# Kernel optimization log

Measured on AMD Instinct MI355X. Metric: run time of the kernel, lower is better.

The kernel has to match this reference:

```python
import jax, jax.numpy as jnp
import numpy as np

B, S, DIM, NL = 8, 1024, 1024, 2
EPS = 1e-5
# FeedForward hidden: int(2*(4*DIM)/3)=2730 -> round to multiple_of=256 -> 2816
FFN_HID = 2816


def _uniform(key, shape, k):
    return jax.random.uniform(key, shape, jnp.float32, -k, k)


def setup_inputs() -> dict:
    key = jax.random.key(0)
    ks = jax.random.split(key, 16)
    k = 1.0 / np.sqrt(DIM)
    inp = {
        'x': jax.random.normal(ks[0], (B, S, DIM), jnp.float32),
        'gru_norm_w': jnp.ones((DIM,), jnp.float32),
        # layer 0: input size DIM; layer 1: input size 2*DIM (bidirectional concat)
        'w_ih_l0': _uniform(ks[1], (2, 3 * DIM, DIM), k),
        'w_hh_l0': _uniform(ks[2], (2, 3 * DIM, DIM), k),
        'b_ih_l0': _uniform(ks[3], (2, 3 * DIM), k),
        'b_hh_l0': _uniform(ks[4], (2, 3 * DIM), k),
        'w_ih_l1': _uniform(ks[5], (2, 3 * DIM, 2 * DIM), k),
        'w_hh_l1': _uniform(ks[6], (2, 3 * DIM, DIM), k),
        'b_ih_l1': _uniform(ks[7], (2, 3 * DIM), k),
        'b_hh_l1': _uniform(ks[8], (2, 3 * DIM), k),
        'gru_out_w': _uniform(ks[9], (DIM, 2 * DIM), 1.0 / np.sqrt(2 * DIM)),
        'ffn_norm_w': jnp.ones((DIM,), jnp.float32),
        'w1': _uniform(ks[10], (FFN_HID, DIM), k),
        'w2': _uniform(ks[11], (DIM, FFN_HID), 1.0 / np.sqrt(FFN_HID)),
        'w3': _uniform(ks[12], (FFN_HID, DIM), k),
    }
    return inp


def rmsnorm(x, w, eps=EPS):
    return x * jax.lax.rsqrt(jnp.mean(x * x, axis=-1, keepdims=True) + eps) * w


def gru_dir(x, w_ih, w_hh, b_ih, b_hh, reverse):
    """One GRU direction. x: [B,S,Din] -> [B,S,H]. PyTorch gate order r,z,n."""
    H = w_hh.shape[1]
    # precompute input gates for all timesteps (big GEMM)
    xg = jnp.einsum('bsd,gd->bsg', x, w_ih) + b_ih        # [B,S,3H]
    xg = jnp.swapaxes(xg, 0, 1)                            # [S,B,3H]
    h0 = jnp.zeros((x.shape[0], H), x.dtype)

    def step(h, g):
        hg = h @ w_hh.T + b_hh                             # [B,3H]
        xr, xz, xn = jnp.split(g, 3, axis=-1)
        hr, hz, hn = jnp.split(hg, 3, axis=-1)
        r = jax.nn.sigmoid(xr + hr)
        z = jax.nn.sigmoid(xz + hz)
        n = jnp.tanh(xn + r * hn)
        h = (1.0 - z) * n + z * h
        return h, h

    _, ys = jax.lax.scan(step, h0, xg, reverse=reverse)    # outputs in input order
    return jnp.swapaxes(ys, 0, 1)                          # [B,S,H]


def reference(x, gru_norm_w, w_ih_l0, w_hh_l0, b_ih_l0, b_hh_l0,
              w_ih_l1, w_hh_l1, b_ih_l1, b_hh_l1,
              gru_out_w, ffn_norm_w, w1, w2, w3):
    h = rmsnorm(x, gru_norm_w)
    for wi, wh, bi, bh in ((w_ih_l0, w_hh_l0, b_ih_l0, b_hh_l0),
                           (w_ih_l1, w_hh_l1, b_ih_l1, b_hh_l1)):
        fwd = gru_dir(h, wi[0], wh[0], bi[0], bh[0], reverse=False)
        bwd = gru_dir(h, wi[1], wh[1], bi[1], bh[1], reverse=True)
        h = jnp.concatenate([fwd, bwd], axis=-1)           # [B,S,2*DIM]
    x = x + h @ gru_out_w.T                                # residual 1
    hn = rmsnorm(x, ffn_norm_w)
    ffn = (jax.nn.silu(hn @ w1.T) * (hn @ w3.T)) @ w2.T    # SwiGLU
    return x + ffn                                         # residual 2
```

## Files before the change

kernel.cpp:

```cpp
#include <hip/hip_runtime.h>
#include <stdint.h>


#define S_LEN 1024
#define NWG_DIR 64
#define HPW 16
#define WSTR 1032

typedef __attribute__((ext_vector_type(8))) __bf16 bf16x8;
typedef __attribute__((ext_vector_type(4))) float f32x4;

__device__ __forceinline__ float bf2f(unsigned short u) {
    union { unsigned int i; float f; } v; v.i = ((unsigned int)u) << 16; return v.f;
}
__device__ __forceinline__ unsigned short f2bf(float f) {
    unsigned int i = __float_as_uint(f);
    unsigned int r = (i + 0x7fffu + ((i >> 16) & 1u)) >> 16;
    return (unsigned short)r;
}
__device__ __forceinline__ bool dt_is_f32(const unsigned int* dt) {
    return dt[0] == 0x3F800000u;
}
__device__ __forceinline__ float ld_ext(const void* p, long i, bool f32) {
    return f32 ? ((const float*)p)[i] : bf2f(((const unsigned short*)p)[i]);
}
__device__ __forceinline__ void st8bf(unsigned short* d, float4 a, float4 b) {
    uint4 u;
    u.x = (unsigned)f2bf(a.x) | ((unsigned)f2bf(a.y) << 16);
    u.y = (unsigned)f2bf(a.z) | ((unsigned)f2bf(a.w) << 16);
    u.z = (unsigned)f2bf(b.x) | ((unsigned)f2bf(b.y) << 16);
    u.w = (unsigned)f2bf(b.z) | ((unsigned)f2bf(b.w) << 16);
    *(uint4*)d = u;
}
__device__ __forceinline__ void gload_lds16(const void* g, void* l) {
    __builtin_amdgcn_global_load_lds(
        (const __attribute__((address_space(1))) unsigned int*)g,
        (__attribute__((address_space(3))) unsigned int*)l, 16, 0, 0);
}
__device__ __forceinline__ unsigned int a_ld32(const unsigned int* p) {
    return __hip_atomic_load(p, __ATOMIC_RELAXED, __HIP_MEMORY_SCOPE_AGENT);
}
__device__ __forceinline__ unsigned long long a_ld64(const unsigned long long* p) {
    return __hip_atomic_load(p, __ATOMIC_RELAXED, __HIP_MEMORY_SCOPE_AGENT);
}
__device__ __forceinline__ void a_st32(unsigned int* p, unsigned int v) {
    __hip_atomic_store(p, v, __ATOMIC_RELAXED, __HIP_MEMORY_SCOPE_AGENT);
}

template <bool EXT_IN>
__global__ __launch_bounds__(256) void rmsnorm_k(const void* __restrict__ xin,
                                                 const void* __restrict__ w,
                                                 unsigned short* __restrict__ outp,
                                                 const unsigned int* __restrict__ dt) {
    const bool f32 = dt_is_f32(dt);
    const long row = blockIdx.x;
    const int tid = threadIdx.x;
    float v[4];
    if (!EXT_IN || f32) {
        const float* x = (const float*)xin + row * 1024 + tid * 4;
        f32x4 f = *(const f32x4*)x;
        v[0] = f[0]; v[1] = f[1]; v[2] = f[2]; v[3] = f[3];
    } else {
        const unsigned short* x = (const unsigned short*)xin + row * 1024 + tid * 4;
        uint2 u = *(const uint2*)x;
        v[0] = bf2f((unsigned short)(u.x & 0xffff)); v[1] = bf2f((unsigned short)(u.x >> 16));
        v[2] = bf2f((unsigned short)(u.y & 0xffff)); v[3] = bf2f((unsigned short)(u.y >> 16));
    }
    float ss = v[0]*v[0] + v[1]*v[1] + v[2]*v[2] + v[3]*v[3];
    for (int off = 32; off > 0; off >>= 1) ss += __shfl_down(ss, off, 64);
    __shared__ float red[4];
    __shared__ float bc;
    if ((tid & 63) == 0) red[tid >> 6] = ss;
    __syncthreads();
    if (tid == 0) bc = rsqrtf((red[0] + red[1] + red[2] + red[3]) * (1.f / 1024.f) + 1e-5f);
    __syncthreads();
    const float sc = bc;
    unsigned short o0 = f2bf(v[0] * sc * ld_ext(w, tid*4+0, f32));
    unsigned short o1 = f2bf(v[1] * sc * ld_ext(w, tid*4+1, f32));
    unsigned short o2 = f2bf(v[2] * sc * ld_ext(w, tid*4+2, f32));
    unsigned short o3 = f2bf(v[3] * sc * ld_ext(w, tid*4+3, f32));
    *(uint2*)(outp + row * 1024 + tid * 4) =
        make_uint2((unsigned int)o0 | ((unsigned int)o1 << 16),
                   (unsigned int)o2 | ((unsigned int)o3 << 16));
}

enum { EPI_NONE = 0, EPI_SILU = 1, EPI_MUL_I = 2, EPI_ADD_EXT = 3, EPI_ADD_F32 = 4 };
enum { OUT_BF16 = 0, OUT_F32 = 1, OUT_EXT = 2 };

template <int EPI, int OUTMODE, bool HAS_BIAS>
__global__ __launch_bounds__(256) void gemm_bt(const unsigned short* __restrict__ A,
                                               const void* __restrict__ W,
                                               const void* __restrict__ bias,
                                               const void* __restrict__ aux,
                                               void* __restrict__ Cout, int N, int K,
                                               const unsigned int* __restrict__ dt) {
    __shared__ __align__(16) unsigned short sA[128 * 32];
    __shared__ __align__(16) unsigned short sB[128 * 32];
    const bool f32 = dt_is_f32(dt);
    const int tid = threadIdx.x;
    const int lane = tid & 63;
    const int wave = tid >> 6;
    const int wm = (wave >> 1) * 64, wn = (wave & 1) * 64;
    const int lm = lane & 15, q = lane >> 4;
    const long rowA0 = (long)blockIdx.y * 128;
    const long rowB0 = (long)blockIdx.x * 128;
    const int r0 = tid >> 2, c0 = tid & 3;

    f32x4 acc[4][4] = {};

    for (int kt = 0; kt < K; kt += 32) {
        gload_lds16(A + (rowA0 + r0) * K + kt + c0 * 8, &sA[tid * 8]);
        gload_lds16(A + (rowA0 + r0 + 64) * K + kt + c0 * 8, &sA[(tid + 256) * 8]);
        if (!f32) {
            const unsigned short* Wb = (const unsigned short*)W;
            gload_lds16(Wb + (rowB0 + r0) * K + kt + c0 * 8, &sB[tid * 8]);
            gload_lds16(Wb + (rowB0 + r0 + 64) * K + kt + c0 * 8, &sB[(tid + 256) * 8]);
        } else {
            const float* Wf = (const float*)W;
            const float* p0 = Wf + (rowB0 + r0) * K + kt + c0 * 8;
            const float* p1 = Wf + (rowB0 + r0 + 64) * K + kt + c0 * 8;
            float4 a0 = *(const float4*)p0, a1 = *(const float4*)(p0 + 4);
            float4 b0 = *(const float4*)p1, b1 = *(const float4*)(p1 + 4);
            st8bf(&sB[tid * 8], a0, a1);
            st8bf(&sB[(tid + 256) * 8], b0, b1);
        }
        __syncthreads();
        bf16x8 af[4], bfr[4];
#pragma unroll
        for (int i = 0; i < 4; ++i) af[i] = *(const bf16x8*)&sA[(wm + i * 16 + lm) * 32 + q * 8];
#pragma unroll
        for (int j = 0; j < 4; ++j) bfr[j] = *(const bf16x8*)&sB[(wn + j * 16 + lm) * 32 + q * 8];
#pragma unroll
        for (int i = 0; i < 4; ++i)
#pragma unroll
            for (int j = 0; j < 4; ++j)
                acc[i][j] = __builtin_amdgcn_mfma_f32_16x16x32_bf16(af[i], bfr[j], acc[i][j], 0, 0, 0);
        __syncthreads();
    }

#pragma unroll
    for (int j = 0; j < 4; ++j) {
        const long col = rowB0 + wn + j * 16 + lm;
        float bv = 0.f;
        if (HAS_BIAS) bv = ld_ext(bias, col, f32);
#pragma unroll
        for (int i = 0; i < 4; ++i) {
#pragma unroll
            for (int r = 0; r < 4; ++r) {
                const long row = rowA0 + wm + i * 16 + q * 4 + r;
                const long idx = row * N + col;
                float v = acc[i][j][r] + bv;
                if (EPI == EPI_SILU)    v = v / (1.f + __expf(-v));
                if (EPI == EPI_MUL_I)   v *= bf2f(((const unsigned short*)aux)[idx]);
                if (EPI == EPI_ADD_EXT) v += ld_ext(aux, idx, f32);
                if (EPI == EPI_ADD_F32) v += ((const float*)aux)[idx];
                if (OUTMODE == OUT_F32)       ((float*)Cout)[idx] = v;
                else if (OUTMODE == OUT_BF16) ((unsigned short*)Cout)[idx] = f2bf(v);
                else { if (f32) ((float*)Cout)[idx] = v; else ((unsigned short*)Cout)[idx] = f2bf(v); }
            }
        }
    }
}

__global__ __launch_bounds__(256) void gru_recur(const unsigned short* __restrict__ xg,
                                                 const void* __restrict__ whh,
                                                 const void* __restrict__ bhh,
                                                 unsigned short* __restrict__ out,
                                                 unsigned short* __restrict__ hpp,
                                                 unsigned int* __restrict__ flags,
                                                 const unsigned int* __restrict__ dt) {
    extern __shared__ char smem[];
    unsigned short* w_lds = (unsigned short*)smem;
    unsigned short* h_lds = w_lds + 48 * WSTR;
    float* xg_lds = (float*)(h_lds + 16 * WSTR);
    float* red = xg_lds + 768;
    float* hstate = red + 3072;
    float* bhh_l = hstate + 128;
    unsigned short* hpub = (unsigned short*)(bhh_l + 48);

    const bool f32 = dt_is_f32(dt);
    const int tid = threadIdx.x;
    const int lane = tid & 63, wave = tid >> 6;
    const int dir = blockIdx.x >> 6;
    const int slot = blockIdx.x & 63;
    const int H0 = slot * HPW;
    const int lm = lane & 15, q = lane >> 4;
    unsigned int* fl = flags + dir * 64;

    for (int idx = tid; idx < 48 * 128; idx += 256) {
        int row = idx >> 7, seg = idx & 127;
        int gate = row >> 4, j = row & 15;
        size_t grow = (size_t)(dir * 3072 + gate * 1024 + H0 + j);
        if (!f32) {
            uint4 vv = *(const uint4*)((const unsigned short*)whh + grow * 1024 + seg * 8);
            *(uint4*)&w_lds[row * WSTR + seg * 8] = vv;
        } else {
            const float* wf = (const float*)whh + grow * 1024 + seg * 8;
            float4 a = *(const float4*)wf, b = *(const float4*)(wf + 4);
            st8bf(&w_lds[row * WSTR + seg * 8], a, b);
        }
    }
    if (tid < 48) {
        int gate = tid >> 4, j = tid & 15;
        bhh_l[tid] = ld_ext(bhh, dir * 3072 + gate * 1024 + H0 + j, f32);
    }
    if (tid < 128) hstate[tid] = 0.f;
    for (int i = tid; i < 16 * 128; i += 256) {
        int m = i >> 7, sg = i & 127;
        uint4 z = {0, 0, 0, 0};
        *(uint4*)&h_lds[m * WSTR + sg * 8] = z;
    }
    {
        int s0 = dir ? (S_LEN - 1) : 0;
        if (tid < 192) {
            int v0 = tid * 2, m = v0 / 48, c = v0 % 48;
            int gate = c >> 4, j = c & 15;
            unsigned int u = *(const unsigned int*)(xg + (size_t)(m * S_LEN + s0) * 6144 +
                                                   dir * 3072 + gate * 1024 + H0 + j);
            xg_lds[m * 48 + c] = bf2f((unsigned short)(u & 0xffff));
            xg_lds[m * 48 + c + 1] = bf2f((unsigned short)(u >> 16));
        }
    }

    unsigned short* hpp_d = hpp + (size_t)dir * 2 * 8 * 1024;
    unsigned int* hpp_u32 = (unsigned int*)hpp_d;
    const unsigned long long* hpp_u64 = (const unsigned long long*)hpp_d;

    for (int t = 0; t < S_LEN; ++t) {
        const int s = dir ? (S_LEN - 1 - t) : t;
        const int buf = t & 1;

        unsigned int nxt = 0;
        int nm = 0, nc = 0;
        const bool has_nxt = (t + 1 < S_LEN) && (tid < 192);
        if (has_nxt) {
            int sn = dir ? (S_LEN - 2 - t) : (t + 1);
            int v0 = tid * 2; nm = v0 / 48; nc = v0 % 48;
            int gate = nc >> 4, j = nc & 15;
            nxt = *(const unsigned int*)(xg + (size_t)(nm * S_LEN + sn) * 6144 +
                                         dir * 3072 + gate * 1024 + H0 + j);
        }
        if (t > 0) {
            if (wave == 0) {
                unsigned int f;
                do {
                    f = a_ld32(&fl[lane]);
                } while (__ballot(f < (unsigned int)t) != 0ULL);
            }
            __syncthreads();
            const unsigned long long* src = hpp_u64 + (size_t)((t - 1) & 1) * 2048;
#pragma unroll
            for (int i = 0; i < 8; ++i) {
                int idx = tid + i * 256;
                int m = idx >> 8, qw = idx & 255;
                unsigned long long v = a_ld64(src + m * 256 + qw);
                *(unsigned long long*)&h_lds[m * WSTR + qw * 4] = v;
            }
        }
        if (has_nxt) {
            xg_lds[(buf ^ 1) * 384 + nm * 48 + nc] = bf2f((unsigned short)(nxt & 0xffff));
            xg_lds[(buf ^ 1) * 384 + nm * 48 + nc + 1] = bf2f((unsigned short)(nxt >> 16));
        }
        __syncthreads();
        f32x4 pacc[3] = {};
#pragma unroll
        for (int kk = 0; kk < 8; ++kk) {
            const int k0 = (wave * 8 + kk) * 32 + q * 8;
            bf16x8 a = *(const bf16x8*)&h_lds[lm * WSTR + k0];
#pragma unroll
            for (int tl = 0; tl < 3; ++tl) {
                bf16x8 b = *(const bf16x8*)&w_lds[(tl * 16 + lm) * WSTR + k0];
                pacc[tl] = __builtin_amdgcn_mfma_f32_16x16x32_bf16(a, b, pacc[tl], 0, 0, 0);
            }
        }
#pragma unroll
        for (int tl = 0; tl < 3; ++tl)
            *(f32x4*)&red[((wave * 3 + tl) * 64 + lane) * 4] = pacc[tl];
        __syncthreads();
        if (tid < 128) {
            const int m = tid >> 4, hh = tid & 15;
            const int cl = (m >> 2) * 16 + hh, rg = m & 3;
            float rp = 0.f, zp = 0.f, np = 0.f;
#pragma unroll
            for (int wv = 0; wv < 4; ++wv) {
                rp += red[((wv * 3 + 0) * 64 + cl) * 4 + rg];
                zp += red[((wv * 3 + 1) * 64 + cl) * 4 + rg];
                np += red[((wv * 3 + 2) * 64 + cl) * 4 + rg];
            }
            const float* xb = &xg_lds[buf * 384 + m * 48];
            float rr = xb[hh] + rp + bhh_l[hh];
            float zz = xb[16 + hh] + zp + bhh_l[16 + hh];
            float hn_ = np + bhh_l[32 + hh];
            float rgate = 1.f / (1.f + __expf(-rr));
            float zgate = 1.f / (1.f + __expf(-zz));
            float ngate = tanhf(xb[32 + hh] + rgate * hn_);
            float hv = (1.f - zgate) * ngate + zgate * hstate[tid];
            hstate[tid] = hv;
            unsigned short hb = f2bf(hv);
            hpub[tid] = hb;
            out[(size_t)(m * S_LEN + s) * 2048 + dir * 1024 + H0 + hh] = hb;
        }
        __syncthreads();
        if (wave == 0) {
            unsigned int hw = *(const unsigned int*)&hpub[lane * 2];
            int m = lane >> 3, j = lane & 7;
            a_st32(hpp_u32 + ((size_t)buf * 8 + m) * 512 + (H0 >> 1) + j, hw);
            asm volatile("s_waitcnt vmcnt(0)" ::: "memory");
            if (lane == 0) a_st32(&fl[slot], (unsigned int)(t + 1));
        }
    }
}

extern "C" void kernel_launch(void* const* d_in, const int* in_sizes, int n_in,
                              void* d_out, int out_size, void* d_ws, size_t ws_size,
                              hipStream_t stream) {
    (void)in_sizes; (void)n_in; (void)out_size; (void)ws_size;
    const void* x    = d_in[0];
    const unsigned int* dt = (const unsigned int*)d_in[1];
    const void* gnw  = d_in[1];
    const void* wih0 = d_in[2];
    const void* whh0 = d_in[3];
    const void* bih0 = d_in[4];
    const void* bhh0 = d_in[5];
    const void* wih1 = d_in[6];
    const void* whh1 = d_in[7];
    const void* bih1 = d_in[8];
    const void* bhh1 = d_in[9];
    const void* gow  = d_in[10];
    const void* fnw  = d_in[11];
    const void* w1   = d_in[12];
    const void* w2   = d_in[13];
    const void* w3   = d_in[14];

    char* ws = (char*)d_ws;
    size_t o = 0;
    auto alloc = [&](size_t b) { size_t r = o; o += (b + 255) & ~(size_t)255; return r; };
    const size_t oFLG = alloc(2 * 2 * 64 * 4);
    const size_t oHPP = alloc((size_t)2 * 2 * 8 * 1024 * 2);
    const size_t oHN  = alloc((size_t)8192 * 1024 * 2);
    const size_t oXG  = alloc((size_t)8192 * 6144 * 2);
    const size_t oG0  = alloc((size_t)8192 * 2048 * 2);
    const size_t oG1  = alloc((size_t)8192 * 2048 * 2);

    unsigned int* flg    = (unsigned int*)(ws + oFLG);
    unsigned short* hpp  = (unsigned short*)(ws + oHPP);
    unsigned short* hnrm = (unsigned short*)(ws + oHN);
    unsigned short* xg   = (unsigned short*)(ws + oXG);
    unsigned short* g0   = (unsigned short*)(ws + oG0);
    unsigned short* g1   = (unsigned short*)(ws + oG1);
    unsigned short* act  = xg;
    unsigned short* gbuf = xg + (size_t)8192 * 2816;
    float* x1            = (float*)(ws + oG0);

    const size_t lds = (size_t)(48 + 16) * WSTR * 2 + (768 + 3072 + 128 + 48) * 4 + 256;
    (void)hipFuncSetAttribute(reinterpret_cast<const void*>(&gru_recur),
                              hipFuncAttributeMaxDynamicSharedMemorySize, (int)lds);

    hipMemsetAsync(ws + oFLG, 0, 2 * 2 * 64 * 4, stream);
    rmsnorm_k<true><<<8192, 256, 0, stream>>>(x, gnw, hnrm, dt);
    gemm_bt<EPI_NONE, OUT_BF16, true><<<dim3(48, 64), 256, 0, stream>>>(hnrm, wih0, bih0, nullptr, xg, 6144, 1024, dt);
    gru_recur<<<128, 256, lds, stream>>>(xg, whh0, bhh0, g0, hpp, flg, dt);
    gemm_bt<EPI_NONE, OUT_BF16, true><<<dim3(48, 64), 256, 0, stream>>>(g0, wih1, bih1, nullptr, xg, 6144, 2048, dt);
    gru_recur<<<128, 256, lds, stream>>>(xg, whh1, bhh1, g1, hpp, flg + 128, dt);
    gemm_bt<EPI_ADD_EXT, OUT_F32, false><<<dim3(8, 64), 256, 0, stream>>>(g1, gow, nullptr, x, x1, 1024, 2048, dt);
    rmsnorm_k<false><<<8192, 256, 0, stream>>>(x1, fnw, hnrm, dt);
    gemm_bt<EPI_SILU, OUT_BF16, false><<<dim3(22, 64), 256, 0, stream>>>(hnrm, w1, nullptr, nullptr, act, 2816, 1024, dt);
    gemm_bt<EPI_MUL_I, OUT_BF16, false><<<dim3(22, 64), 256, 0, stream>>>(hnrm, w3, nullptr, act, gbuf, 2816, 1024, dt);
    gemm_bt<EPI_ADD_F32, OUT_EXT, false><<<dim3(8, 64), 256, 0, stream>>>(gbuf, w2, nullptr, x1, d_out, 1024, 2816, dt);
}
```

Before: 10.45 ms.

## Replace GRU flag barrier with checksum-validated hidden-state publication and register-held weights

The persistent GRU recurrence no longer publishes hidden-state slices plus a separate per-workgroup flag that a waiting wave polls. Each workgroup now writes its slice together with a step-keyed hash, and readers spin until the hash matches, so one round-trip replaces a flag wait followed by a data load. W_hh fragments are also preloaded into registers instead of being read from LDS every step, tanh switches to an exp-based form, and the output store moves to a second wave. This cuts latency on the serial critical path, but the checksum scheme carries a small risk of false validation and the extra registers may cause spilling.

```diff
diff --git a/kernel.cpp b/kernel.cpp
--- a/kernel.cpp
+++ b/kernel.cpp
@@ -3,9 +3,9 @@
 
 
 #define S_LEN 1024
-#define NWG_DIR 64
 #define HPW 16
 #define WSTR 1032
+#define HASH_K 0x9E3779B1u
 
 typedef __attribute__((ext_vector_type(8))) __bf16 bf16x8;
 typedef __attribute__((ext_vector_type(4))) float f32x4;
@@ -45,6 +45,13 @@
 }
 __device__ __forceinline__ void a_st32(unsigned int* p, unsigned int v) {
     __hip_atomic_store(p, v, __ATOMIC_RELAXED, __HIP_MEMORY_SCOPE_AGENT);
+}
+__device__ __forceinline__ unsigned int rotl32(unsigned int x, int s) {
+    return (x << s) | (x >> ((32 - s) & 31));
+}
+__device__ __forceinline__ float fast_tanh(float x) {
+    float ex = __expf(2.f * x);
+    return 1.f - 2.f / (ex + 1.f);
 }
 
 template <bool EXT_IN>
@@ -162,13 +169,12 @@
     }
 }
 
-__global__ __launch_bounds__(256) void gru_recur(const unsigned short* __restrict__ xg,
-                                                 const void* __restrict__ whh,
-                                                 const void* __restrict__ bhh,
-                                                 unsigned short* __restrict__ out,
-                                                 unsigned short* __restrict__ hpp,
-                                                 unsigned int* __restrict__ flags,
-                                                 const unsigned int* __restrict__ dt) {
+__global__ __launch_bounds__(256, 1) void gru_recur(const unsigned short* __restrict__ xg,
+                                                    const void* __restrict__ whh,
+                                                    const void* __restrict__ bhh,
+                                                    unsigned short* __restrict__ out,
+                                                    unsigned int* __restrict__ hpp,
+                                                    const unsigned int* __restrict__ dt) {
     extern __shared__ char smem[];
     unsigned short* w_lds = (unsigned short*)smem;
     unsigned short* h_lds = w_lds + 48 * WSTR;
@@ -185,7 +191,7 @@
     const int slot = blockIdx.x & 63;
     const int H0 = slot * HPW;
     const int lm = lane & 15, q = lane >> 4;
-    unsigned int* fl = flags + dir * 64;
+    unsigned int* hppD = hpp + dir * (2 * 64 * 68);
 
     for (int idx = tid; idx < 48 * 128; idx += 256) {
         int row = idx >> 7, seg = idx & 127;
@@ -221,10 +227,15 @@
             xg_lds[m * 48 + c + 1] = bf2f((unsigned short)(u >> 16));
         }
     }
-
-    unsigned short* hpp_d = hpp + (size_t)dir * 2 * 8 * 1024;
-    unsigned int* hpp_u32 = (unsigned int*)hpp_d;
-    const unsigned long long* hpp_u64 = (const unsigned long long*)hpp_d;
+    __syncthreads();
+    bf16x8 wfrag[8][3];
+#pragma unroll
+    for (int kk = 0; kk < 8; ++kk)
+#pragma unroll
+        for (int tl = 0; tl < 3; ++tl)
+            wfrag[kk][tl] = *(const bf16x8*)&w_lds[(tl * 16 + lm) * WSTR + (wave * 8 + kk) * 32 + q * 8];
+
+    const int cp = tid >> 2, cr = tid & 3;
 
     for (int t = 0; t < S_LEN; ++t) {
         const int s = dir ? (S_LEN - 1 - t) : t;
@@ -241,21 +252,38 @@
                                          dir * 3072 + gate * 1024 + H0 + j);
         }
         if (t > 0) {
-            if (wave == 0) {
-                unsigned int f;
-                do {
-                    f = a_ld32(&fl[lane]);
-                } while (__ballot(f < (unsigned int)t) != 0ULL);
-            }
-            __syncthreads();
-            const unsigned long long* src = hpp_u64 + (size_t)((t - 1) & 1) * 2048;
-#pragma unroll
-            for (int i = 0; i < 8; ++i) {
-                int idx = tid + i * 256;
-                int m = idx >> 8, qw = idx & 255;
-                unsigned long long v = a_ld64(src + m * 256 + qw);
-                *(unsigned long long*)&h_lds[m * WSTR + qw * 4] = v;
-            }
+            const unsigned int hashv = (unsigned int)t * HASH_K;
+            const unsigned int* base = hppD + ((t - 1) & 1) * (64 * 68) + cp * 68;
+            const unsigned long long* srcq = (const unsigned long long*)(base) + cr * 8;
+            unsigned long long d[8];
+            int ok;
+            do {
+#pragma unroll
+                for (int k2 = 0; k2 < 8; ++k2) d[k2] = a_ld64(srcq + k2);
+                unsigned int cs = a_ld32(base + 64);
+                unsigned int x = 0;
+#pragma unroll
+                for (int k2 = 0; k2 < 8; ++k2) {
+                    int i0 = cr * 16 + 2 * k2;
+                    x ^= rotl32((unsigned int)d[k2], i0 & 31) ^
+                         rotl32((unsigned int)(d[k2] >> 32), (i0 + 1) & 31);
+                }
+                unsigned int sx = x ^ __shfl_xor(x, 1);
+                sx ^= __shfl_xor(sx, 2);
+                ok = ((sx ^ hashv) == cs);
+            } while (__syncthreads_count(ok) < 256);
+            uint4 w0 = { (unsigned int)d[0], (unsigned int)(d[0] >> 32),
+                         (unsigned int)d[1], (unsigned int)(d[1] >> 32) };
+            uint4 w1 = { (unsigned int)d[2], (unsigned int)(d[2] >> 32),
+                         (unsigned int)d[3], (unsigned int)(d[3] >> 32) };
+            uint4 w2 = { (unsigned int)d[4], (unsigned int)(d[4] >> 32),
+                         (unsigned int)d[5], (unsigned int)(d[5] >> 32) };
+            uint4 w3 = { (unsigned int)d[6], (unsigned int)(d[6] >> 32),
+                         (unsigned int)d[7], (unsigned int)(d[7] >> 32) };
+            *(uint4*)&h_lds[(cr * 2) * WSTR + cp * 16] = w0;
+            *(uint4*)&h_lds[(cr * 2) * WSTR + cp * 16 + 8] = w1;
+            *(uint4*)&h_lds[(cr * 2 + 1) * WSTR + cp * 16] = w2;
+            *(uint4*)&h_lds[(cr * 2 + 1) * WSTR + cp * 16 + 8] = w3;
         }
         if (has_nxt) {
             xg_lds[(buf ^ 1) * 384 + nm * 48 + nc] = bf2f((unsigned short)(nxt & 0xffff));
@@ -268,10 +296,8 @@
             const int k0 = (wave * 8 + kk) * 32 + q * 8;
             bf16x8 a = *(const bf16x8*)&h_lds[lm * WSTR + k0];
 #pragma unroll
-            for (int tl = 0; tl < 3; ++tl) {
-                bf16x8 b = *(const bf16x8*)&w_lds[(tl * 16 + lm) * WSTR + k0];
-                pacc[tl] = __builtin_amdgcn_mfma_f32_16x16x32_bf16(a, b, pacc[tl], 0, 0, 0);
-            }
+            for (int tl = 0; tl < 3; ++tl)
+                pacc[tl] = __builtin_amdgcn_mfma_f32_16x16x32_bf16(a, wfrag[kk][tl], pacc[tl], 0, 0, 0);
         }
 #pragma unroll
         for (int tl = 0; tl < 3; ++tl)
@@ -293,20 +319,25 @@
             float hn_ = np + bhh_l[32 + hh];
             float rgate = 1.f / (1.f + __expf(-rr));
             float zgate = 1.f / (1.f + __expf(-zz));
-            float ngate = tanhf(xb[32 + hh] + rgate * hn_);
+            float ngate = fast_tanh(xb[32 + hh] + rgate * hn_);
             float hv = (1.f - zgate) * ngate + zgate * hstate[tid];
             hstate[tid] = hv;
-            unsigned short hb = f2bf(hv);
-            hpub[tid] = hb;
-            out[(size_t)(m * S_LEN + s) * 2048 + dir * 1024 + H0 + hh] = hb;
+            hpub[tid] = f2bf(hv);
         }
         __syncthreads();
         if (wave == 0) {
-            unsigned int hw = *(const unsigned int*)&hpub[lane * 2];
-            int m = lane >> 3, j = lane & 7;
-            a_st32(hpp_u32 + ((size_t)buf * 8 + m) * 512 + (H0 >> 1) + j, hw);
-            asm volatile("s_waitcnt vmcnt(0)" ::: "memory");
-            if (lane == 0) a_st32(&fl[slot], (unsigned int)(t + 1));
+            unsigned int dd = *(const unsigned int*)&hpub[lane * 2];
+            unsigned int e = rotl32(dd, lane & 31);
+#pragma unroll
+            for (int off = 1; off < 64; off <<= 1) e ^= __shfl_xor(e, off);
+            unsigned int* pub = hppD + buf * (64 * 68) + slot * 68;
+            a_st32(pub + lane, dd);
+            if (lane == 0) a_st32(pub + 64, e ^ ((unsigned int)(t + 1) * HASH_K));
+        }
+        if (wave == 1) {
+            int i2 = tid - 64, m = i2 >> 3, j = i2 & 7;
+            ((unsigned int*)out)[(size_t)(m * S_LEN + s) * 1024 + dir * 512 + (H0 >> 1) + j] =
+                *(const unsigned int*)&hpub[i2 * 2];
         }
     }
 }
@@ -335,15 +366,13 @@
     char* ws = (char*)d_ws;
     size_t o = 0;
     auto alloc = [&](size_t b) { size_t r = o; o += (b + 255) & ~(size_t)255; return r; };
-    const size_t oFLG = alloc(2 * 2 * 64 * 4);
-    const size_t oHPP = alloc((size_t)2 * 2 * 8 * 1024 * 2);
+    const size_t oHPP = alloc((size_t)2 * 2 * 2 * 64 * 68 * 4);
     const size_t oHN  = alloc((size_t)8192 * 1024 * 2);
     const size_t oXG  = alloc((size_t)8192 * 6144 * 2);
     const size_t oG0  = alloc((size_t)8192 * 2048 * 2);
     const size_t oG1  = alloc((size_t)8192 * 2048 * 2);
 
-    unsigned int* flg    = (unsigned int*)(ws + oFLG);
-    unsigned short* hpp  = (unsigned short*)(ws + oHPP);
+    unsigned int* hpp    = (unsigned int*)(ws + oHPP);
     unsigned short* hnrm = (unsigned short*)(ws + oHN);
     unsigned short* xg   = (unsigned short*)(ws + oXG);
     unsigned short* g0   = (unsigned short*)(ws + oG0);
@@ -356,12 +385,11 @@
     (void)hipFuncSetAttribute(reinterpret_cast<const void*>(&gru_recur),
                               hipFuncAttributeMaxDynamicSharedMemorySize, (int)lds);
 
-    hipMemsetAsync(ws + oFLG, 0, 2 * 2 * 64 * 4, stream);
     rmsnorm_k<true><<<8192, 256, 0, stream>>>(x, gnw, hnrm, dt);
     gemm_bt<EPI_NONE, OUT_BF16, true><<<dim3(48, 64), 256, 0, stream>>>(hnrm, wih0, bih0, nullptr, xg, 6144, 1024, dt);
-    gru_recur<<<128, 256, lds, stream>>>(xg, whh0, bhh0, g0, hpp, flg, dt);
+    gru_recur<<<128, 256, lds, stream>>>(xg, whh0, bhh0, g0, hpp, dt);
     gemm_bt<EPI_NONE, OUT_BF16, true><<<dim3(48, 64), 256, 0, stream>>>(g0, wih1, bih1, nullptr, xg, 6144, 2048, dt);
-    gru_recur<<<128, 256, lds, stream>>>(xg, whh1, bhh1, g1, hpp, flg + 128, dt);
+    gru_recur<<<128, 256, lds, stream>>>(xg, whh1, bhh1, g1, hpp + 2 * 2 * 64 * 68, dt);
     gemm_bt<EPI_ADD_EXT, OUT_F32, false><<<dim3(8, 64), 256, 0, stream>>>(g1, gow, nullptr, x, x1, 1024, 2048, dt);
     rmsnorm_k<false><<<8192, 256, 0, stream>>>(x1, fnw, hnrm, dt);
     gemm_bt<EPI_SILU, OUT_BF16, false><<<dim3(22, 64), 256, 0, stream>>>(hnrm, w1, nullptr, nullptr, act, 2816, 1024, dt);
```

Result: slower. 10.82 ms (+3.5%).
